# Performance work log

Measured on AMD Instinct MI355X. Metric: run time of the kernel, lower is better.

Reference implementation:

```python
import jax, jax.numpy as jnp
import numpy as np
from jax import lax

EPS = 1e-5

def binarize(x):
    # sign() forward, straight-through (identity) backward, like BinarizeConv2d's .data trick
    return x + lax.stop_gradient(jnp.sign(x) - x)

def conv_nchw(x, w, stride, pad):
    return lax.conv_general_dilated(
        x, w, window_strides=(stride, stride), padding=((pad, pad), (pad, pad)),
        dimension_numbers=('NCHW', 'OIHW', 'NCHW'))

def batchnorm_train(x, gamma, beta):
    # training-mode BN: per-channel batch mean / biased variance over (N,H,W)
    mean = jnp.mean(x, axis=(0, 2, 3), keepdims=True)
    var = jnp.mean((x - mean) ** 2, axis=(0, 2, 3), keepdims=True)
    xhat = (x - mean) * lax.rsqrt(var + EPS)
    return xhat * gamma[None, :, None, None] + beta[None, :, None, None]

def hardtanh(x):
    return jnp.clip(x, -1.0, 1.0)

def setup_inputs() -> dict:
    key = jax.random.key(0)
    ks = jax.random.split(key, 7)
    N, Cin, Cout, H, W = 32, 64, 64, 128, 128
    x = jax.random.normal(ks[0], (N, Cin, H, W), dtype=jnp.float32)
    w1 = jax.random.normal(ks[1], (Cout, Cin, 3, 3), dtype=jnp.float32) * 0.05
    w2 = jax.random.normal(ks[2], (Cout, Cout, 3, 3), dtype=jnp.float32) * 0.05
    g1 = jnp.ones((Cout,), dtype=jnp.float32)
    b1 = jnp.zeros((Cout,), dtype=jnp.float32)
    g2 = jnp.ones((Cout,), dtype=jnp.float32)
    b2 = jnp.zeros((Cout,), dtype=jnp.float32)
    return {"x": x, "w1": w1, "g1": g1, "b1": b1, "w2": w2, "g2": g2, "b2": b2}

def reference(x, w1, g1, b1, w2, g2, b2):
    # conv1: binarized input (C=64 != 3) and binarized weights
    out = conv_nchw(binarize(x), binarize(w1), stride=1, pad=1)
    out = hardtanh(batchnorm_train(out, g1, b1))
    # conv2: 3x3, stride 1 (stride==1 branch)
    out = conv_nchw(binarize(out), binarize(w2), stride=1, pad=1)
    out = batchnorm_train(out, g2, b2)
    # identity shortcut (stride==1 and in_planes==planes)
    out = out + x
    return hardtanh(out)
```

## Files before the change

kernel.cpp:

```cpp
#include <hip/hip_runtime.h>
#include <stdint.h>

typedef unsigned long long u64;
typedef unsigned int u32;

#define Nn 32
#define Cc 64
#define Hh 128
#define Ww 128
#define HPAD 130
#define WPAD 130
#define NHW_TOT (Nn*Hh*Ww)
#define NBIN 16

__device__ __forceinline__ float2 compute_ab(const u64* __restrict__ sum, const u64* __restrict__ sq,
        const float* __restrict__ g, const float* __restrict__ bet, int c) {
    long long Sv = 0, Qv = 0;
    #pragma unroll
    for (int b = 0; b < NBIN; ++b) {
        Sv += (long long)sum[b * 64 + c];
        Qv += (long long)sq[b * 64 + c];
    }
    double mean = (double)Sv / (double)NHW_TOT;
    double var = (double)Qv / (double)NHW_TOT - mean * mean;
    double invstd = 1.0 / sqrt(var + 1e-5);
    double a = (double)g[c] * invstd;
    double b_ = (double)bet[c] - a * mean;
    return make_float2((float)a, (float)b_);
}

__global__ __launch_bounds__(256) void pack_x4_kernel(const float* __restrict__ x,
                                                      u64* __restrict__ xpad) {
    int t = blockIdx.x * 256 + threadIdx.x;
    int P = t * 4;
    int row = P >> 7, w0 = P & 127;
    int n = row >> 7, h = row & 127;
    const float4* xp4 = (const float4*)(x + ((size_t)n * Cc * Hh + h) * Ww + w0);
    u32 lo0 = 0, lo1 = 0, lo2 = 0, lo3 = 0, hi0 = 0, hi1 = 0, hi2 = 0, hi3 = 0;
    #pragma unroll 8
    for (int c = 0; c < 32; ++c) {
        float4 v = xp4[c * (Hh * Ww / 4)];
        lo0 |= (__float_as_uint(v.x) >> 31) << c;
        lo1 |= (__float_as_uint(v.y) >> 31) << c;
        lo2 |= (__float_as_uint(v.z) >> 31) << c;
        lo3 |= (__float_as_uint(v.w) >> 31) << c;
    }
    #pragma unroll 8
    for (int c = 32; c < 64; ++c) {
        float4 v = xp4[c * (Hh * Ww / 4)];
        hi0 |= (__float_as_uint(v.x) >> 31) << (c - 32);
        hi1 |= (__float_as_uint(v.y) >> 31) << (c - 32);
        hi2 |= (__float_as_uint(v.z) >> 31) << (c - 32);
        hi3 |= (__float_as_uint(v.w) >> 31) << (c - 32);
    }
    u64* dst = xpad + ((size_t)n * HPAD + h + 1) * WPAD + w0 + 1;
    dst[0] = ((u64)hi0 << 32) | lo0;
    dst[1] = ((u64)hi1 << 32) | lo1;
    dst[2] = ((u64)hi2 << 32) | lo2;
    dst[3] = ((u64)hi3 << 32) | lo3;
}

__global__ __launch_bounds__(576) void pack_w_kernel(
        const float* __restrict__ w1, const float* __restrict__ w2,
        u64* __restrict__ w1b, u64* __restrict__ w2b) {
    int t = threadIdx.x;
    const float* src = blockIdx.x ? w2 : w1;
    u64* db = blockIdx.x ? w2b : w1b;
    int co = t / 9, tap = t - co * 9;
    const float* p = src + (size_t)co * 576 + tap;
    u32 lo = 0, hi = 0;
    #pragma unroll
    for (int ci = 0; ci < 32; ++ci)
        lo |= (__float_as_uint(p[ci * 9]) >> 31) << ci;
    #pragma unroll
    for (int ci = 32; ci < 64; ++ci)
        hi |= (__float_as_uint(p[ci * 9]) >> 31) << (ci - 32);
    db[t] = ((u64)hi << 32) | lo;
}

__device__ __forceinline__ void conv4(const u64* __restrict__ L0, const u64* __restrict__ L1,
                                      const u64* __restrict__ L2, int w,
                                      const u64 W[9], int corrMid, int v[4]) {
    u64 a[6], b[6], c[6];
    #pragma unroll
    for (int j = 0; j < 6; ++j) { a[j] = L0[w + j]; b[j] = L1[w + j]; c[j] = L2[w + j]; }
    #pragma unroll
    for (int px = 0; px < 4; ++px) {
        int p0 = __popcll(a[px] ^ W[0]) + __popcll(a[px + 1] ^ W[1]) + __popcll(a[px + 2] ^ W[2]);
        int p1 = __popcll(b[px] ^ W[3]) + __popcll(b[px + 1] ^ W[4]) + __popcll(b[px + 2] ^ W[5]);
        int p2 = __popcll(c[px] ^ W[6]) + __popcll(c[px + 1] ^ W[7]) + __popcll(c[px + 2] ^ W[8]);
        v[px] = 576 - 2 * (p0 + p1 + p2) - corrMid;
    }
}

struct LaneCtx {
    u64 W[9];
    int corrMid, corrW0, corrW127;
};

__device__ __forceinline__ void lane_setup(LaneCtx& C, const u64* __restrict__ wb,
                                           int lane, int h) {
    #pragma unroll
    for (int t = 0; t < 9; ++t) C.W[t] = wb[lane * 9 + t];
    int wc[9];
    #pragma unroll
    for (int t = 0; t < 9; ++t) wc[t] = 64 - 2 * __popcll(C.W[t]);
    int tT = wc[0] + wc[1] + wc[2], tB = wc[6] + wc[7] + wc[8];
    int tL = wc[0] + wc[3] + wc[6], tR = wc[2] + wc[5] + wc[8];
    bool fT = (h == 0), fB = (h == 127);
    C.corrMid  = (fT ? tT : 0) + (fB ? tB : 0);
    C.corrW0   = tL - (fT ? wc[0] : 0) - (fB ? wc[6] : 0);
    C.corrW127 = tR - (fT ? wc[2] : 0) - (fB ? wc[8] : 0);
}

template<bool SPILL>
__global__ __launch_bounds__(128) void conv_statsT(const u64* __restrict__ inpad,
        const u64* __restrict__ wb, u64* __restrict__ gsum, u64* __restrict__ gsq,
        short* __restrict__ v16) {
    __shared__ u64 win[4 * 68];
    __shared__ int r32[256];
    int tid = threadIdx.x;
    int lane = tid & 63;
    int wv = __builtin_amdgcn_readfirstlane(tid >> 6);
    int blk = blockIdx.x;
    int half = blk & 1;
    int hp = (blk >> 1) & 63;
    int n = blk >> 7;
    int h = hp * 2 + wv;
    const u64* src = inpad + ((size_t)n * HPAD + hp * 2) * WPAD + half * 64;
    for (int i = tid; i < 264; i += 128) {
        int r = i / 66, c = i - r * 66;
        win[r * 68 + c] = src[(size_t)r * WPAD + c];
    }
    LaneCtx C;
    lane_setup(C, wb, lane, h);
    __syncthreads();
    const u64* L0 = &win[wv * 68];
    const u64* L1 = L0 + 68;
    const u64* L2 = L0 + 136;
    short* vrow = SPILL ? (v16 + (((size_t)(n * Hh + h) * Ww) + half * 64) * 64 + lane) : nullptr;
    int s = 0, q = 0;
    for (int w = 0; w < 64; w += 4) {
        int v[4];
        conv4(L0, L1, L2, w, C.W, C.corrMid, v);
        if (half == 0 && w == 0)  v[0] -= C.corrW0;
        if (half == 1 && w == 60) v[3] -= C.corrW127;
        #pragma unroll
        for (int px = 0; px < 4; ++px) {
            s += v[px];
            q += __mul24(v[px], v[px]);
            if (SPILL) vrow[(size_t)(w + px) * 64] = (short)v[px];
        }
    }
    __syncthreads();
    r32[wv * 64 + lane] = s;
    r32[128 + wv * 64 + lane] = q;
    __syncthreads();
    if (wv == 0) {
        int S = r32[lane] + r32[64 + lane];
        int Q = r32[128 + lane] + r32[192 + lane];
        int bin = blk & (NBIN - 1);
        atomicAdd(&gsum[bin * 64 + lane], (u64)(long long)S);
        atomicAdd(&gsq[bin * 64 + lane], (u64)(long long)Q);
    }
}

__global__ __launch_bounds__(256) void signpack_v(const short* __restrict__ v16,
        const u64* __restrict__ sum, const u64* __restrict__ sq,
        const float* __restrict__ g, const float* __restrict__ bet,
        u64* __restrict__ ypad) {
    int tid = threadIdx.x;
    int lane = tid & 63;
    int wv = tid >> 6;
    int grow = blockIdx.x * 2 + (wv >> 1);
    int base = (wv & 1) * 64;
    int n = grow >> 7, h = grow & 127;
    float2 ab = compute_ab(sum, sq, g, bet, lane);
    const short* vr = v16 + ((size_t)grow * Ww + base) * 64;
    u64* drow = ypad + ((size_t)n * HPAD + h + 1) * WPAD + 1;
    u64 myw = 0;
    #pragma unroll 8
    for (int px = 0; px < 64; ++px) {
        float tv = fmaf((float)vr[(size_t)px * 64 + lane], ab.x, ab.y);
        u64 bal = __ballot(tv < 0.0f);
        if (lane == px) myw = bal;
    }
    drow[base + lane] = myw;
}

__global__ __launch_bounds__(256) void signpack_rc(const u64* __restrict__ inpad,
        const u64* __restrict__ wb, const u64* __restrict__ sum, const u64* __restrict__ sq,
        const float* __restrict__ g, const float* __restrict__ bet,
        u64* __restrict__ outpad) {
    __shared__ u64 win[6 * 130];
    int tid = threadIdx.x;
    int lane = tid & 63;
    int wv = __builtin_amdgcn_readfirstlane(tid >> 6);
    int blk = blockIdx.x;
    int n = blk >> 5, hb = (blk & 31) << 2;
    int h = hb + wv;
    const u64* src = inpad + ((size_t)n * HPAD + hb) * WPAD;
    for (int i = tid; i < 780; i += 256) win[i] = src[i];
    LaneCtx C;
    lane_setup(C, wb, lane, h);
    float2 ab = compute_ab(sum, sq, g, bet, lane);
    __syncthreads();
    const u64* L0 = &win[wv * 130];
    const u64* L1 = L0 + 130;
    const u64* L2 = L0 + 260;
    u64* drow = outpad + ((size_t)n * HPAD + h + 1) * WPAD + 1;
    for (int w = 0; w < 128; w += 4) {
        int v[4];
        conv4(L0, L1, L2, w, C.W, C.corrMid, v);
        if (w == 0)   v[0] -= C.corrW0;
        if (w == 124) v[3] -= C.corrW127;
        u64 wd[4];
        #pragma unroll
        for (int px = 0; px < 4; ++px) {
            float t = fmaf((float)v[px], ab.x, ab.y);
            wd[px] = __ballot(t < 0.0f);
        }
        if (lane == 0) {
            drow[w] = wd[0]; drow[w + 1] = wd[1]; drow[w + 2] = wd[2]; drow[w + 3] = wd[3];
        }
    }
}

__global__ __launch_bounds__(128) void final5_kernel(const u64* __restrict__ inpad,
        const u64* __restrict__ wb, const u64* __restrict__ sum, const u64* __restrict__ sq,
        const float* __restrict__ g, const float* __restrict__ bet,
        const float* __restrict__ x, float* __restrict__ out) {
    __shared__ u64 win[4 * 68];
    __shared__ short T[2][64 * 36];
    __shared__ float2 absh[64];
    int tid = threadIdx.x;
    int lane = tid & 63;
    int wv = __builtin_amdgcn_readfirstlane(tid >> 6);
    int blk = blockIdx.x;
    int half = blk & 1;
    int hp = (blk >> 1) & 63;
    int n = blk >> 7;
    int h = hp * 2 + wv;
    const u64* src = inpad + ((size_t)n * HPAD + hp * 2) * WPAD + half * 64;
    for (int i = tid; i < 264; i += 128) {
        int r = i / 66, c = i - r * 66;
        win[r * 68 + c] = src[(size_t)r * WPAD + c];
    }
    LaneCtx C;
    lane_setup(C, wb, lane, h);
    if (tid < 64) absh[tid] = compute_ab(sum, sq, g, bet, tid);
    __syncthreads();
    const u64* L0 = &win[wv * 68];
    const u64* L1 = L0 + 68;
    const u64* L2 = L0 + 136;
    short* Tw = T[wv];
    int p4 = lane & 7;
    int cosub = lane >> 3;
    size_t base_nch = ((size_t)n * Cc * Hh + h) * Ww;
    for (int w = 0; w < 64; w += 4) {
        int v[4];
        conv4(L0, L1, L2, w, C.W, C.corrMid, v);
        if (half == 0 && w == 0)  v[0] -= C.corrW0;
        if (half == 1 && w == 60) v[3] -= C.corrW127;
        short4 sv;
        sv.x = (short)v[0]; sv.y = (short)v[1]; sv.z = (short)v[2]; sv.w = (short)v[3];
        *(short4*)&Tw[lane * 36 + (w & 31)] = sv;
        if ((w & 31) == 28) {
            int w0g = half * 64 + (w & ~31);
            #pragma unroll 8
            for (int st = 0; st < 8; ++st) {
                int co = st * 8 + cosub;
                short4 tv = *(const short4*)&Tw[co * 36 + p4 * 4];
                float2 cab = absh[co];
                size_t idx = base_nch + (size_t)co * (Hh * Ww) + w0g + p4 * 4;
                float4 xv = *(const float4*)(x + idx);
                float4 yv;
                yv.x = fminf(1.0f, fmaxf(-1.0f, fmaf((float)tv.x, cab.x, cab.y) + xv.x));
                yv.y = fminf(1.0f, fmaxf(-1.0f, fmaf((float)tv.y, cab.x, cab.y) + xv.y));
                yv.z = fminf(1.0f, fmaxf(-1.0f, fmaf((float)tv.z, cab.x, cab.y) + xv.z));
                yv.w = fminf(1.0f, fmaxf(-1.0f, fmaf((float)tv.w, cab.x, cab.y) + xv.w));
                *(float4*)(out + idx) = yv;
            }
        }
    }
}

extern "C" void kernel_launch(void* const* d_in, const int* in_sizes, int n_in,
                              void* d_out, int out_size, void* d_ws, size_t ws_size,
                              hipStream_t stream) {
    const float* x  = (const float*)d_in[0];
    const float* w1 = (const float*)d_in[1];
    const float* g1 = (const float*)d_in[2];
    const float* b1 = (const float*)d_in[3];
    const float* w2 = (const float*)d_in[4];
    const float* g2 = (const float*)d_in[5];
    const float* b2 = (const float*)d_in[6];
    float* out = (float*)d_out;
    char* ws = (char*)d_ws;

    constexpr size_t SZ_PAD   = (size_t)Nn * HPAD * WPAD * sizeof(u64);
    constexpr size_t OFF_YPAD = SZ_PAD;
    constexpr size_t OFF_STAT = 2 * SZ_PAD;
    constexpr size_t SZ_STAT  = (size_t)NBIN * 64 * 8;
    constexpr size_t OFF_W1B  = OFF_STAT + 4 * SZ_STAT;
    constexpr size_t OFF_W2B  = OFF_W1B + 576 * 8;
    constexpr size_t OFF_V16  = OFF_W2B + 576 * 8;
    constexpr size_t SZ_V16   = (size_t)Nn * Hh * Ww * 64 * 2;
    constexpr size_t WS_SMALL = OFF_V16;
    constexpr size_t WS_FULL  = OFF_V16 + SZ_V16;

    if (ws_size < WS_SMALL) return;
    bool spill = (ws_size >= WS_FULL);

    u64* xpad = (u64*)(ws);
    u64* ypad = (u64*)(ws + OFF_YPAD);
    u64* gsum1 = (u64*)(ws + OFF_STAT);
    u64* gsq1  = (u64*)(ws + OFF_STAT + SZ_STAT);
    u64* gsum2 = (u64*)(ws + OFF_STAT + 2 * SZ_STAT);
    u64* gsq2  = (u64*)(ws + OFF_STAT + 3 * SZ_STAT);
    u64* w1b  = (u64*)(ws + OFF_W1B);
    u64* w2b  = (u64*)(ws + OFF_W2B);
    short* v16 = (short*)(ws + OFF_V16);

    hipMemsetAsync(ws, 0, 2 * SZ_PAD + 4 * SZ_STAT, stream);

    pack_x4_kernel<<<512, 256, 0, stream>>>(x, xpad);
    pack_w_kernel<<<2, 576, 0, stream>>>(w1, w2, w1b, w2b);
    if (spill) {
        conv_statsT<true><<<4096, 128, 0, stream>>>(xpad, w1b, gsum1, gsq1, v16);
        signpack_v<<<2048, 256, 0, stream>>>(v16, gsum1, gsq1, g1, b1, ypad);
    } else {
        conv_statsT<false><<<4096, 128, 0, stream>>>(xpad, w1b, gsum1, gsq1, nullptr);
        signpack_rc<<<1024, 256, 0, stream>>>(xpad, w1b, gsum1, gsq1, g1, b1, ypad);
    }
    conv_statsT<false><<<4096, 128, 0, stream>>>(ypad, w2b, gsum2, gsq2, nullptr);
    final5_kernel<<<4096, 128, 0, stream>>>(ypad, w2b, gsum2, gsq2, g2, b2, x, out);
}
```

Baseline: 221.7 us.

## Fuse prep kernels, zero only borders, recompute conv1 instead of spilling int16

Merges the x-pack and weight-pack kernels into one launch, which also zeroes only the padding borders of xpad/ypad and the stats buffers, replacing a full-workspace memset. Drops the int16 spill path for conv1 outputs and always recomputes conv1 in a new half-row signpack kernel that matches the conv_stats tiling. This removes a large memset and a big intermediate write/read at the cost of recomputing the binary convolution.

```diff
diff --git a/kernel.cpp b/kernel.cpp
--- a/kernel.cpp
+++ b/kernel.cpp
@@ -29,53 +29,79 @@
     return make_float2((float)a, (float)b_);
 }
 
-__global__ __launch_bounds__(256) void pack_x4_kernel(const float* __restrict__ x,
-                                                      u64* __restrict__ xpad) {
-    int t = blockIdx.x * 256 + threadIdx.x;
-    int P = t * 4;
-    int row = P >> 7, w0 = P & 127;
-    int n = row >> 7, h = row & 127;
-    const float4* xp4 = (const float4*)(x + ((size_t)n * Cc * Hh + h) * Ww + w0);
-    u32 lo0 = 0, lo1 = 0, lo2 = 0, lo3 = 0, hi0 = 0, hi1 = 0, hi2 = 0, hi3 = 0;
-    #pragma unroll 8
-    for (int c = 0; c < 32; ++c) {
-        float4 v = xp4[c * (Hh * Ww / 4)];
-        lo0 |= (__float_as_uint(v.x) >> 31) << c;
-        lo1 |= (__float_as_uint(v.y) >> 31) << c;
-        lo2 |= (__float_as_uint(v.z) >> 31) << c;
-        lo3 |= (__float_as_uint(v.w) >> 31) << c;
-    }
-    #pragma unroll 8
-    for (int c = 32; c < 64; ++c) {
-        float4 v = xp4[c * (Hh * Ww / 4)];
-        hi0 |= (__float_as_uint(v.x) >> 31) << (c - 32);
-        hi1 |= (__float_as_uint(v.y) >> 31) << (c - 32);
-        hi2 |= (__float_as_uint(v.z) >> 31) << (c - 32);
-        hi3 |= (__float_as_uint(v.w) >> 31) << (c - 32);
-    }
-    u64* dst = xpad + ((size_t)n * HPAD + h + 1) * WPAD + w0 + 1;
-    dst[0] = ((u64)hi0 << 32) | lo0;
-    dst[1] = ((u64)hi1 << 32) | lo1;
-    dst[2] = ((u64)hi2 << 32) | lo2;
-    dst[3] = ((u64)hi3 << 32) | lo3;
-}
-
-__global__ __launch_bounds__(576) void pack_w_kernel(
+#define BORDER_PER_IMG 516
+#define BORDER_TOT (Nn * BORDER_PER_IMG)
+#define PREP_EXTRA (1152 + 2 * BORDER_TOT + 4 * NBIN * 64)
+
+__global__ __launch_bounds__(256) void prep_kernel(const float* __restrict__ x,
         const float* __restrict__ w1, const float* __restrict__ w2,
-        u64* __restrict__ w1b, u64* __restrict__ w2b) {
-    int t = threadIdx.x;
-    const float* src = blockIdx.x ? w2 : w1;
-    u64* db = blockIdx.x ? w2b : w1b;
-    int co = t / 9, tap = t - co * 9;
-    const float* p = src + (size_t)co * 576 + tap;
-    u32 lo = 0, hi = 0;
-    #pragma unroll
-    for (int ci = 0; ci < 32; ++ci)
-        lo |= (__float_as_uint(p[ci * 9]) >> 31) << ci;
-    #pragma unroll
-    for (int ci = 32; ci < 64; ++ci)
-        hi |= (__float_as_uint(p[ci * 9]) >> 31) << (ci - 32);
-    db[t] = ((u64)hi << 32) | lo;
+        u64* __restrict__ xpad, u64* __restrict__ ypad,
+        u64* __restrict__ w1b, u64* __restrict__ w2b, u64* __restrict__ stats) {
+    if (blockIdx.x < 512) {
+        int t = blockIdx.x * 256 + threadIdx.x;
+        int P = t * 4;
+        int row = P >> 7, w0 = P & 127;
+        int n = row >> 7, h = row & 127;
+        const float4* xp4 = (const float4*)(x + ((size_t)n * Cc * Hh + h) * Ww + w0);
+        u32 lo0 = 0, lo1 = 0, lo2 = 0, lo3 = 0, hi0 = 0, hi1 = 0, hi2 = 0, hi3 = 0;
+        #pragma unroll 8
+        for (int c = 0; c < 32; ++c) {
+            float4 v = xp4[c * (Hh * Ww / 4)];
+            lo0 |= (__float_as_uint(v.x) >> 31) << c;
+            lo1 |= (__float_as_uint(v.y) >> 31) << c;
+            lo2 |= (__float_as_uint(v.z) >> 31) << c;
+            lo3 |= (__float_as_uint(v.w) >> 31) << c;
+        }
+        #pragma unroll 8
+        for (int c = 32; c < 64; ++c) {
+            float4 v = xp4[c * (Hh * Ww / 4)];
+            hi0 |= (__float_as_uint(v.x) >> 31) << (c - 32);
+            hi1 |= (__float_as_uint(v.y) >> 31) << (c - 32);
+            hi2 |= (__float_as_uint(v.z) >> 31) << (c - 32);
+            hi3 |= (__float_as_uint(v.w) >> 31) << (c - 32);
+        }
+        u64* dst = xpad + ((size_t)n * HPAD + h + 1) * WPAD + w0 + 1;
+        dst[0] = ((u64)hi0 << 32) | lo0;
+        dst[1] = ((u64)hi1 << 32) | lo1;
+        dst[2] = ((u64)hi2 << 32) | lo2;
+        dst[3] = ((u64)hi3 << 32) | lo3;
+    } else {
+        int t = (blockIdx.x - 512) * 256 + threadIdx.x;
+        int stride = (gridDim.x - 512) * 256;
+        for (int i = t; i < PREP_EXTRA; i += stride) {
+            if (i < 1152) {
+                int set = i / 576, idx = i - set * 576;
+                const float* src = set ? w2 : w1;
+                u64* db = set ? w2b : w1b;
+                int co = idx / 9, tap = idx - co * 9;
+                const float* p = src + (size_t)co * 576 + tap;
+                u32 lo = 0, hi = 0;
+                #pragma unroll
+                for (int ci = 0; ci < 32; ++ci)
+                    lo |= (__float_as_uint(p[ci * 9]) >> 31) << ci;
+                #pragma unroll
+                for (int ci = 32; ci < 64; ++ci)
+                    hi |= (__float_as_uint(p[ci * 9]) >> 31) << (ci - 32);
+                db[idx] = ((u64)hi << 32) | lo;
+            } else if (i < 1152 + 2 * BORDER_TOT) {
+                int z = i - 1152;
+                u64* buf = (z < BORDER_TOT) ? xpad : ypad;
+                int k = (z < BORDER_TOT) ? z : z - BORDER_TOT;
+                int img = k / BORDER_PER_IMG, j = k - img * BORDER_PER_IMG;
+                size_t base = (size_t)img * HPAD * WPAD;
+                size_t off;
+                if (j < 130)      off = j;
+                else if (j < 260) off = (size_t)(HPAD - 1) * WPAD + (j - 130);
+                else {
+                    int k2 = j - 260;
+                    off = (size_t)(1 + (k2 >> 1)) * WPAD + ((k2 & 1) ? (WPAD - 1) : 0);
+                }
+                buf[base + off] = 0ull;
+            } else {
+                stats[i - 1152 - 2 * BORDER_TOT] = 0ull;
+            }
+        }
+    }
 }
 
 __device__ __forceinline__ void conv4(const u64* __restrict__ L0, const u64* __restrict__ L1,
@@ -113,10 +139,17 @@
     C.corrW127 = tR - (fT ? wc[2] : 0) - (fB ? wc[8] : 0);
 }
 
-template<bool SPILL>
-__global__ __launch_bounds__(128) void conv_statsT(const u64* __restrict__ inpad,
-        const u64* __restrict__ wb, u64* __restrict__ gsum, u64* __restrict__ gsq,
-        short* __restrict__ v16) {
+__device__ __forceinline__ void load_win(u64* __restrict__ win, const u64* __restrict__ inpad,
+                                         int n, int hp, int half, int tid) {
+    const u64* src = inpad + ((size_t)n * HPAD + hp * 2) * WPAD + half * 64;
+    for (int i = tid; i < 264; i += 128) {
+        int r = i / 66, c = i - r * 66;
+        win[r * 68 + c] = src[(size_t)r * WPAD + c];
+    }
+}
+
+__global__ __launch_bounds__(128) void conv_stats(const u64* __restrict__ inpad,
+        const u64* __restrict__ wb, u64* __restrict__ gsum, u64* __restrict__ gsq) {
     __shared__ u64 win[4 * 68];
     __shared__ int r32[256];
     int tid = threadIdx.x;
@@ -127,18 +160,13 @@
     int hp = (blk >> 1) & 63;
     int n = blk >> 7;
     int h = hp * 2 + wv;
-    const u64* src = inpad + ((size_t)n * HPAD + hp * 2) * WPAD + half * 64;
-    for (int i = tid; i < 264; i += 128) {
-        int r = i / 66, c = i - r * 66;
-        win[r * 68 + c] = src[(size_t)r * WPAD + c];
-    }
+    load_win(win, inpad, n, hp, half, tid);
     LaneCtx C;
     lane_setup(C, wb, lane, h);
     __syncthreads();
     const u64* L0 = &win[wv * 68];
     const u64* L1 = L0 + 68;
     const u64* L2 = L0 + 136;
-    short* vrow = SPILL ? (v16 + (((size_t)(n * Hh + h) * Ww) + half * 64) * 64 + lane) : nullptr;
     int s = 0, q = 0;
     for (int w = 0; w < 64; w += 4) {
         int v[4];
@@ -149,7 +177,6 @@
         for (int px = 0; px < 4; ++px) {
             s += v[px];
             q += __mul24(v[px], v[px]);
-            if (SPILL) vrow[(size_t)(w + px) * 64] = (short)v[px];
         }
     }
     __syncthreads();
@@ -165,65 +192,41 @@
     }
 }
 
-__global__ __launch_bounds__(256) void signpack_v(const short* __restrict__ v16,
-        const u64* __restrict__ sum, const u64* __restrict__ sq,
+__global__ __launch_bounds__(128) void signpack_h(const u64* __restrict__ inpad,
+        const u64* __restrict__ wb, const u64* __restrict__ sum, const u64* __restrict__ sq,
         const float* __restrict__ g, const float* __restrict__ bet,
         u64* __restrict__ ypad) {
-    int tid = threadIdx.x;
-    int lane = tid & 63;
-    int wv = tid >> 6;
-    int grow = blockIdx.x * 2 + (wv >> 1);
-    int base = (wv & 1) * 64;
-    int n = grow >> 7, h = grow & 127;
-    float2 ab = compute_ab(sum, sq, g, bet, lane);
-    const short* vr = v16 + ((size_t)grow * Ww + base) * 64;
-    u64* drow = ypad + ((size_t)n * HPAD + h + 1) * WPAD + 1;
-    u64 myw = 0;
-    #pragma unroll 8
-    for (int px = 0; px < 64; ++px) {
-        float tv = fmaf((float)vr[(size_t)px * 64 + lane], ab.x, ab.y);
-        u64 bal = __ballot(tv < 0.0f);
-        if (lane == px) myw = bal;
-    }
-    drow[base + lane] = myw;
-}
-
-__global__ __launch_bounds__(256) void signpack_rc(const u64* __restrict__ inpad,
-        const u64* __restrict__ wb, const u64* __restrict__ sum, const u64* __restrict__ sq,
-        const float* __restrict__ g, const float* __restrict__ bet,
-        u64* __restrict__ outpad) {
-    __shared__ u64 win[6 * 130];
+    __shared__ u64 win[4 * 68];
     int tid = threadIdx.x;
     int lane = tid & 63;
     int wv = __builtin_amdgcn_readfirstlane(tid >> 6);
     int blk = blockIdx.x;
-    int n = blk >> 5, hb = (blk & 31) << 2;
-    int h = hb + wv;
-    const u64* src = inpad + ((size_t)n * HPAD + hb) * WPAD;
-    for (int i = tid; i < 780; i += 256) win[i] = src[i];
+    int half = blk & 1;
+    int hp = (blk >> 1) & 63;
+    int n = blk >> 7;
+    int h = hp * 2 + wv;
+    load_win(win, inpad, n, hp, half, tid);
     LaneCtx C;
     lane_setup(C, wb, lane, h);
     float2 ab = compute_ab(sum, sq, g, bet, lane);
     __syncthreads();
-    const u64* L0 = &win[wv * 130];
-    const u64* L1 = L0 + 130;
-    const u64* L2 = L0 + 260;
-    u64* drow = outpad + ((size_t)n * HPAD + h + 1) * WPAD + 1;
-    for (int w = 0; w < 128; w += 4) {
+    const u64* L0 = &win[wv * 68];
+    const u64* L1 = L0 + 68;
+    const u64* L2 = L0 + 136;
+    u64 myw = 0;
+    for (int w = 0; w < 64; w += 4) {
         int v[4];
         conv4(L0, L1, L2, w, C.W, C.corrMid, v);
-        if (w == 0)   v[0] -= C.corrW0;
-        if (w == 124) v[3] -= C.corrW127;
-        u64 wd[4];
+        if (half == 0 && w == 0)  v[0] -= C.corrW0;
+        if (half == 1 && w == 60) v[3] -= C.corrW127;
         #pragma unroll
         for (int px = 0; px < 4; ++px) {
             float t = fmaf((float)v[px], ab.x, ab.y);
-            wd[px] = __ballot(t < 0.0f);
-        }
-        if (lane == 0) {
-            drow[w] = wd[0]; drow[w + 1] = wd[1]; drow[w + 2] = wd[2]; drow[w + 3] = wd[3];
-        }
-    }
+            u64 bal = __ballot(t < 0.0f);
+            if (lane == w + px) myw = bal;
+        }
+    }
+    ypad[((size_t)n * HPAD + h + 1) * WPAD + 1 + half * 64 + lane] = myw;
 }
 
 __global__ __launch_bounds__(128) void final5_kernel(const u64* __restrict__ inpad,
@@ -241,11 +244,7 @@
     int hp = (blk >> 1) & 63;
     int n = blk >> 7;
     int h = hp * 2 + wv;
-    const u64* src = inpad + ((size_t)n * HPAD + hp * 2) * WPAD + half * 64;
-    for (int i = tid; i < 264; i += 128) {
-        int r = i / 66, c = i - r * 66;
-        win[r * 68 + c] = src[(size_t)r * WPAD + c];
-    }
+    load_win(win, inpad, n, hp, half, tid);
     LaneCtx C;
     lane_setup(C, wb, lane, h);
     if (tid < 64) absh[tid] = compute_ab(sum, sq, g, bet, tid);
@@ -304,35 +303,23 @@
     constexpr size_t SZ_STAT  = (size_t)NBIN * 64 * 8;
     constexpr size_t OFF_W1B  = OFF_STAT + 4 * SZ_STAT;
     constexpr size_t OFF_W2B  = OFF_W1B + 576 * 8;
-    constexpr size_t OFF_V16  = OFF_W2B + 576 * 8;
-    constexpr size_t SZ_V16   = (size_t)Nn * Hh * Ww * 64 * 2;
-    constexpr size_t WS_SMALL = OFF_V16;
-    constexpr size_t WS_FULL  = OFF_V16 + SZ_V16;
-
-    if (ws_size < WS_SMALL) return;
-    bool spill = (ws_size >= WS_FULL);
+    constexpr size_t WS_NEEDED = OFF_W2B + 576 * 8;
+
+    if (ws_size < WS_NEEDED) return;
 
     u64* xpad = (u64*)(ws);
     u64* ypad = (u64*)(ws + OFF_YPAD);
+    u64* stats = (u64*)(ws + OFF_STAT);
     u64* gsum1 = (u64*)(ws + OFF_STAT);
     u64* gsq1  = (u64*)(ws + OFF_STAT + SZ_STAT);
     u64* gsum2 = (u64*)(ws + OFF_STAT + 2 * SZ_STAT);
     u64* gsq2  = (u64*)(ws + OFF_STAT + 3 * SZ_STAT);
     u64* w1b  = (u64*)(ws + OFF_W1B);
     u64* w2b  = (u64*)(ws + OFF_W2B);
-    short* v16 = (short*)(ws + OFF_V16);
-
-    hipMemsetAsync(ws, 0, 2 * SZ_PAD + 4 * SZ_STAT, stream);
-
-    pack_x4_kernel<<<512, 256, 0, stream>>>(x, xpad);
-    pack_w_kernel<<<2, 576, 0, stream>>>(w1, w2, w1b, w2b);
-    if (spill) {
-        conv_statsT<true><<<4096, 128, 0, stream>>>(xpad, w1b, gsum1, gsq1, v16);
-        signpack_v<<<2048, 256, 0, stream>>>(v16, gsum1, gsq1, g1, b1, ypad);
-    } else {
-        conv_statsT<false><<<4096, 128, 0, stream>>>(xpad, w1b, gsum1, gsq1, nullptr);
-        signpack_rc<<<1024, 256, 0, stream>>>(xpad, w1b, gsum1, gsq1, g1, b1, ypad);
-    }
-    conv_statsT<false><<<4096, 128, 0, stream>>>(ypad, w2b, gsum2, gsq2, nullptr);
+
+    prep_kernel<<<530, 256, 0, stream>>>(x, w1, w2, xpad, ypad, w1b, w2b, stats);
+    conv_stats<<<4096, 128, 0, stream>>>(xpad, w1b, gsum1, gsq1);
+    signpack_h<<<4096, 128, 0, stream>>>(xpad, w1b, gsum1, gsq1, g1, b1, ypad);
+    conv_stats<<<4096, 128, 0, stream>>>(ypad, w2b, gsum2, gsq2);
     final5_kernel<<<4096, 128, 0, stream>>>(ypad, w2b, gsum2, gsq2, g2, b2, x, out);
 }
```

New measurement: 234.0 us. 1.06x slower.
